# Optimization experiments

Measured on AMD Instinct MI355X. Metric: run time of the kernel, lower is better.

Reference implementation:

```python
import jax, jax.numpy as jnp
import numpy as np

B, D, U = 4096, 2048, 2048

def hard_sigmoid(x):
    # keras hard_sigmoid: clip(0.2*x + 0.5, 0, 1)
    return jnp.clip(0.2 * x + 0.5, 0.0, 1.0)

def setup_inputs() -> dict:
    key = jax.random.key(0)
    k1, k2, k3, k4, k5 = jax.random.split(key, 5)
    return {
        "inputs": jax.random.normal(k1, (B, D), dtype=jnp.float32),
        "h_tm1": jax.random.normal(k2, (B, U), dtype=jnp.float32),
        "c_tm1": jax.random.normal(k3, (B, U), dtype=jnp.float32),
        "kernel": jax.random.normal(k4, (D, 4 * U), dtype=jnp.float32) * 0.02,
        "recurrent_kernel": jax.random.normal(k5, (U, 4 * U), dtype=jnp.float32) * 0.02,
    }

def reference(inputs, h_tm1, c_tm1, kernel, recurrent_kernel):
    u = kernel.shape[1] // 4
    # One fused GEMM each for input and recurrent paths (same math as 8 split GEMMs)
    z = inputs @ kernel + h_tm1 @ recurrent_kernel  # [B, 4U]
    z_i, z_f, z_c, z_o = jnp.split(z, 4, axis=1)
    i = hard_sigmoid(z_i)
    f = hard_sigmoid(z_f)
    c = f * c_tm1 + i * jnp.tanh(z_c)
    o = hard_sigmoid(z_o)
    h = o * jnp.tanh(c)
    return (h, h, c)
```

## Files before the change

### kernel.cpp

```cpp
#include <hip/hip_runtime.h>
#include <stdint.h>

typedef unsigned short u16;
typedef float f32x4 __attribute__((ext_vector_type(4)));
typedef __bf16 bf16x8 __attribute__((ext_vector_type(8)));

#define B_ 4096
#define D_ 2048
#define U_ 2048
#define K_ 4096
#define N_ 8192
#define NT_ 128

__device__ __forceinline__ u16 f32_bf16(float f) {
  uint32_t u = __float_as_uint(f);
  u += 0x7FFFu + ((u >> 16) & 1u);
  return (u16)(u >> 16);
}
__device__ __forceinline__ float hsig(float x) {
  return fminf(fmaxf(0.2f * x + 0.5f, 0.0f), 1.0f);
}
__device__ __forceinline__ float ftanh(float x) {
  x = fminf(fmaxf(x, -15.0f), 15.0f);
  float e = __expf(2.0f * x);
  return (e - 1.0f) / (e + 1.0f);
}
__device__ __forceinline__ void gload16(const void* g, void* l) {
  __builtin_amdgcn_global_load_lds(
      (const __attribute__((address_space(1))) void*)g,
      (__attribute__((address_space(3))) void*)l,
      16, 0, 0);
}

__global__ __launch_bounds__(256) void cast_a(const float* __restrict__ x,
                                              const float* __restrict__ h,
                                              u16* __restrict__ A) {
  int c = blockIdx.x * 256 + threadIdx.x;
  int m = c >> 9;
  int kc = (c & 511) << 3;
  const float* src = (kc < D_) ? (x + (size_t)m * D_ + kc)
                               : (h + (size_t)m * U_ + (kc - D_));
  float4 v0 = ((const float4*)src)[0];
  float4 v1 = ((const float4*)src)[1];
  u16 o[8] = { f32_bf16(v0.x), f32_bf16(v0.y), f32_bf16(v0.z), f32_bf16(v0.w),
               f32_bf16(v1.x), f32_bf16(v1.y), f32_bf16(v1.z), f32_bf16(v1.w) };
  *(uint4*)(A + (size_t)c * 8) = *(const uint4*)o;
}

__global__ __launch_bounds__(256) void cast_wt(const float* __restrict__ kern,
                                               const float* __restrict__ rker,
                                               u16* __restrict__ Wt) {
  __shared__ u16 sW[64][68];
  const int t = threadIdx.x;
  const int bx = blockIdx.x;
  const int by = blockIdx.y;
  const int k0 = by * 64;
  const float* src = (k0 < D_) ? kern : rker;
  const int krow0 = (k0 < D_) ? k0 : (k0 - D_);
#pragma unroll
  for (int i = 0; i < 4; ++i) {
    int c = i * 256 + t;
    int kl = c >> 4;
    int nq = c & 15;
    int g  = nq >> 2;
    int ul = (nq & 3) << 2;
    int n  = g * U_ + bx * 16 + ul;
    float4 v = *(const float4*)(src + (size_t)(krow0 + kl) * N_ + n);
    u16 p[4] = { f32_bf16(v.x), f32_bf16(v.y), f32_bf16(v.z), f32_bf16(v.w) };
    *(ushort4*)&sW[kl][g * 16 + ul] = *(const ushort4*)p;
  }
  __syncthreads();
#pragma unroll
  for (int j = 0; j < 2; ++j) {
    int c2 = j * 256 + t;
    int nl = c2 >> 3;
    int kc = c2 & 7;
    u16 p[8];
#pragma unroll
    for (int jj = 0; jj < 8; ++jj) p[jj] = sW[kc * 8 + jj][nl];
    *(uint4*)(Wt + ((size_t)bx * 64 + nl) * K_ + k0 + kc * 8) = *(const uint4*)p;
  }
}

#define LDSA(par) ((par) * 32768)
#define LDSB(par) ((par) * 32768 + 16384)

#define STAGE4(par, t) do { \
  const u16* ga_ = Ab + (size_t)grow * K_ + (t) * 32 + gch8; \
  const u16* gb_ = Bb + (size_t)grow * K_ + (t) * 32 + gch8; \
  char* la_ = ldsc + LDSA(par) + wid * 1024; \
  char* lb_ = ldsc + LDSB(par) + wid * 1024; \
  gload16(ga_, la_); \
  gload16(ga_ + (size_t)128 * K_, la_ + 8192); \
  gload16(gb_, lb_); \
  gload16(gb_ + (size_t)128 * K_, lb_ + 8192); \
} while (0)

#define VMW(n) asm volatile("s_waitcnt vmcnt(" #n ")" ::: "memory")
#define MFMA16 __builtin_amdgcn_mfma_f32_16x16x32_bf16

#define PHASE(par, STAGE_STMT, VMW_STMT) do { \
  const char* pa_ = ldsc + LDSA(par) + aob; \
  const char* pb_ = ldsc + LDSB(par) + bob; \
  _Pragma("unroll") \
  for (int m_ = 0; m_ < 8; ++m_) av[m_] = *(const bf16x8*)(pa_ + m_ * 1024); \
  _Pragma("unroll") \
  for (int n_ = 0; n_ < 4; ++n_) bv[n_] = *(const bf16x8*)(pb_ + n_ * 1024); \
  STAGE_STMT; \
  VMW_STMT; \
  __builtin_amdgcn_s_barrier(); \
  asm volatile("s_waitcnt lgkmcnt(0)" ::: "memory"); \
  __builtin_amdgcn_sched_barrier(0); \
  __builtin_amdgcn_s_setprio(1); \
  _Pragma("unroll") \
  for (int m_ = 0; m_ < 8; ++m_) { \
    _Pragma("unroll") \
    for (int n_ = 0; n_ < 4; ++n_) \
      acc[m_][n_] = MFMA16(av[m_], bv[n_], acc[m_][n_], 0, 0, 0); \
  } \
  __builtin_amdgcn_s_setprio(0); \
} while (0)

__global__ __launch_bounds__(512, 2) void lstm_gemm(const u16* __restrict__ A,
                                                    const u16* __restrict__ Wt,
                                                    const float* __restrict__ c_prev,
                                                    float* __restrict__ out) {
  __shared__ __align__(16) u16 lds[65536];
  char* ldsc = (char*)lds;
  const int tid  = threadIdx.x;
  const int lane = tid & 63;
  const int wid  = tid >> 6;
  const int wr   = wid >> 2;
  const int wcn  = wid & 3;
  const int fr   = lane & 15;
  const int fq   = lane >> 4;

  const int orig = blockIdx.x;
  const int wg   = ((orig & 7) << 6) | (orig >> 3);
  const int bm   = wg & 15;
  const int bn   = wg >> 4;

  const u16* Ab = A  + (size_t)bm * 256 * K_;
  const u16* Bb = Wt + (size_t)bn * 256 * K_;

  const int grow = tid >> 2;
  const int gch8 = (((tid & 3) ^ ((grow >> 1) & 3)) << 3);
  const int csw = (fq ^ ((fr >> 1) & 3)) << 4;
  const int aob = (wr * 128 + fr) * 64 + csw;
  const int bob = (wcn * 64 + fr) * 64 + csw;

  f32x4 acc[8][4] = {};
  bf16x8 av[8], bv[4];

  STAGE4(0, 0);
  STAGE4(1, 1);
  VMW(4);
  __builtin_amdgcn_s_barrier();

  for (int tb = 0; tb < NT_; tb += 4) {
    PHASE(0, { STAGE4(2, tb + 2); }, { VMW(4); });
    PHASE(1, { STAGE4(3, tb + 3); }, { VMW(4); });
    PHASE(2, { if (tb + 4 < NT_) STAGE4(0, tb + 4); },
          { if (tb + 4 < NT_) { VMW(4); } else { VMW(0); } });
    PHASE(3, { if (tb + 5 < NT_) STAGE4(1, tb + 5); },
          { if (tb + 5 < NT_) { VMW(4); } });
  }

  const int u  = (bn * 4 + wcn) * 16 + fr;
  const size_t BU = (size_t)B_ * U_;
#pragma unroll
  for (int mi = 0; mi < 8; ++mi) {
#pragma unroll
    for (int r = 0; r < 4; ++r) {
      int row = bm * 256 + wr * 128 + mi * 16 + fq * 4 + r;
      float zi = acc[mi][0][r], zf = acc[mi][1][r];
      float zc = acc[mi][2][r], zo = acc[mi][3][r];
      float iv = hsig(zi), fv = hsig(zf), ov = hsig(zo);
      size_t off = (size_t)row * U_ + u;
      float cp = c_prev[off];
      float cv = fv * cp + iv * ftanh(zc);
      float hv = ov * ftanh(cv);
      out[off]          = hv;
      out[BU + off]     = hv;
      out[2 * BU + off] = cv;
    }
  }
}

extern "C" void kernel_launch(void* const* d_in, const int* in_sizes, int n_in,
                              void* d_out, int out_size, void* d_ws, size_t ws_size,
                              hipStream_t stream) {
  const float* x  = (const float*)d_in[0];
  const float* h  = (const float*)d_in[1];
  const float* cp = (const float*)d_in[2];
  const float* kk = (const float*)d_in[3];
  const float* rk = (const float*)d_in[4];
  float* out = (float*)d_out;

  const size_t bytesA  = (size_t)B_ * K_ * 2;
  const size_t bytesWt = (size_t)N_ * K_ * 2;
  if (ws_size < bytesA + bytesWt) return;

  u16* Aws = (u16*)d_ws;
  u16* Wt  = (u16*)((char*)d_ws + bytesA);

  cast_a<<<(B_ * K_ / 8) / 256, 256, 0, stream>>>(x, h, Aws);
  cast_wt<<<dim3(N_ / 64, K_ / 64), 256, 0, stream>>>(kk, rk, Wt);
  lstm_gemm<<<dim3(512), dim3(512), 0, stream>>>(Aws, Wt, cp, out);
}
```

Before: 305.7 us.

## Retile LSTM GEMM to 128x256 blocks with 4 waves and triple-buffered LDS

The GEMM block tile changes from 256x256 with 8 waves to 128x256 with 4 waves, launching 1024 blocks of 256 threads. Each wave now computes a 64x128 tile holding 32-wide gate slices, and cast_wt is rewritten to produce the matching 128-column gate interleave. The LDS pipeline moves from four buffers to three, with the barrier placed at the start of each phase and the LDS wait after the MFMAs. This aims to raise occupancy and overlap LDS reads with compute, at the cost of more A-tile reloads and more total blocks.

```diff
diff --git a/kernel.cpp b/kernel.cpp
--- a/kernel.cpp
+++ b/kernel.cpp
@@ -50,7 +50,7 @@
 __global__ __launch_bounds__(256) void cast_wt(const float* __restrict__ kern,
                                                const float* __restrict__ rker,
                                                u16* __restrict__ Wt) {
-  __shared__ u16 sW[64][68];
+  __shared__ u16 sW[64][134];
   const int t = threadIdx.x;
   const int bx = blockIdx.x;
   const int by = blockIdx.y;
@@ -58,131 +58,142 @@
   const float* src = (k0 < D_) ? kern : rker;
   const int krow0 = (k0 < D_) ? k0 : (k0 - D_);
 #pragma unroll
-  for (int i = 0; i < 4; ++i) {
-    int c = i * 256 + t;
-    int kl = c >> 4;
-    int nq = c & 15;
-    int g  = nq >> 2;
-    int ul = (nq & 3) << 2;
-    int n  = g * U_ + bx * 16 + ul;
+  for (int i = 0; i < 8; ++i) {
+    int q  = i * 256 + t;
+    int kl = q >> 5;
+    int cc = q & 31;
+    int g  = cc >> 3;
+    int n  = g * U_ + bx * 32 + (cc & 7) * 4;
     float4 v = *(const float4*)(src + (size_t)(krow0 + kl) * N_ + n);
     u16 p[4] = { f32_bf16(v.x), f32_bf16(v.y), f32_bf16(v.z), f32_bf16(v.w) };
-    *(ushort4*)&sW[kl][g * 16 + ul] = *(const ushort4*)p;
+    *(ushort4*)&sW[kl][cc * 4] = *(const ushort4*)p;
   }
   __syncthreads();
 #pragma unroll
-  for (int j = 0; j < 2; ++j) {
+  for (int j = 0; j < 4; ++j) {
     int c2 = j * 256 + t;
-    int nl = c2 >> 3;
+    int r  = c2 >> 3;
     int kc = c2 & 7;
     u16 p[8];
 #pragma unroll
-    for (int jj = 0; jj < 8; ++jj) p[jj] = sW[kc * 8 + jj][nl];
-    *(uint4*)(Wt + ((size_t)bx * 64 + nl) * K_ + k0 + kc * 8) = *(const uint4*)p;
-  }
-}
-
-#define LDSA(par) ((par) * 32768)
-#define LDSB(par) ((par) * 32768 + 16384)
-
-#define STAGE4(par, t) do { \
+    for (int jj = 0; jj < 8; ++jj) p[jj] = sW[kc * 8 + jj][r];
+    *(uint4*)(Wt + ((size_t)bx * 128 + r) * K_ + k0 + kc * 8) = *(const uint4*)p;
+  }
+}
+
+#define PA(par) ((par) * 24576)
+#define PB(par) ((par) * 24576 + 8192)
+
+#define STAGE6(par, t) do { \
   const u16* ga_ = Ab + (size_t)grow * K_ + (t) * 32 + gch8; \
   const u16* gb_ = Bb + (size_t)grow * K_ + (t) * 32 + gch8; \
-  char* la_ = ldsc + LDSA(par) + wid * 1024; \
-  char* lb_ = ldsc + LDSB(par) + wid * 1024; \
-  gload16(ga_, la_); \
-  gload16(ga_ + (size_t)128 * K_, la_ + 8192); \
-  gload16(gb_, lb_); \
+  char* la_ = ldsc + PA(par) + wid * 1024; \
+  char* lb_ = ldsc + PB(par) + wid * 1024; \
+  gload16(ga_,                    la_); \
+  gload16(ga_ + (size_t)64 * K_,  la_ + 4096); \
+  gload16(gb_,                    lb_); \
+  gload16(gb_ + (size_t)64 * K_,  lb_ + 4096); \
   gload16(gb_ + (size_t)128 * K_, lb_ + 8192); \
+  gload16(gb_ + (size_t)192 * K_, lb_ + 12288); \
 } while (0)
 
 #define VMW(n) asm volatile("s_waitcnt vmcnt(" #n ")" ::: "memory")
 #define MFMA16 __builtin_amdgcn_mfma_f32_16x16x32_bf16
 
 #define PHASE(par, STAGE_STMT, VMW_STMT) do { \
-  const char* pa_ = ldsc + LDSA(par) + aob; \
-  const char* pb_ = ldsc + LDSB(par) + bob; \
-  _Pragma("unroll") \
-  for (int m_ = 0; m_ < 8; ++m_) av[m_] = *(const bf16x8*)(pa_ + m_ * 1024); \
-  _Pragma("unroll") \
-  for (int n_ = 0; n_ < 4; ++n_) bv[n_] = *(const bf16x8*)(pb_ + n_ * 1024); \
+  __builtin_amdgcn_s_barrier(); \
+  asm volatile("" ::: "memory"); \
+  const char* pa_ = ldsc + PA(par) + aob; \
+  const char* pb_ = ldsc + PB(par) + bob; \
+  av[0] = *(const bf16x8*)(pa_); \
+  bv[0] = *(const bf16x8*)(pb_); \
+  bv[1] = *(const bf16x8*)(pb_ + 1024); \
+  bv[2] = *(const bf16x8*)(pb_ + 2048); \
+  bv[3] = *(const bf16x8*)(pb_ + 3072); \
+  bv[4] = *(const bf16x8*)(pb_ + 4096); \
+  bv[5] = *(const bf16x8*)(pb_ + 5120); \
+  bv[6] = *(const bf16x8*)(pb_ + 6144); \
+  bv[7] = *(const bf16x8*)(pb_ + 7168); \
+  av[1] = *(const bf16x8*)(pa_ + 1024); \
+  av[2] = *(const bf16x8*)(pa_ + 2048); \
+  av[3] = *(const bf16x8*)(pa_ + 3072); \
   STAGE_STMT; \
   VMW_STMT; \
-  __builtin_amdgcn_s_barrier(); \
-  asm volatile("s_waitcnt lgkmcnt(0)" ::: "memory"); \
-  __builtin_amdgcn_sched_barrier(0); \
   __builtin_amdgcn_s_setprio(1); \
   _Pragma("unroll") \
-  for (int m_ = 0; m_ < 8; ++m_) { \
+  for (int m_ = 0; m_ < 4; ++m_) { \
     _Pragma("unroll") \
-    for (int n_ = 0; n_ < 4; ++n_) \
+    for (int n_ = 0; n_ < 8; ++n_) \
       acc[m_][n_] = MFMA16(av[m_], bv[n_], acc[m_][n_], 0, 0, 0); \
   } \
   __builtin_amdgcn_s_setprio(0); \
+  asm volatile("s_waitcnt lgkmcnt(0)" ::: "memory"); \
 } while (0)
 
-__global__ __launch_bounds__(512, 2) void lstm_gemm(const u16* __restrict__ A,
+__global__ __launch_bounds__(256, 2) void lstm_gemm(const u16* __restrict__ A,
                                                     const u16* __restrict__ Wt,
                                                     const float* __restrict__ c_prev,
                                                     float* __restrict__ out) {
-  __shared__ __align__(16) u16 lds[65536];
+  __shared__ __align__(16) u16 lds[36864];
   char* ldsc = (char*)lds;
   const int tid  = threadIdx.x;
   const int lane = tid & 63;
   const int wid  = tid >> 6;
-  const int wr   = wid >> 2;
-  const int wcn  = wid & 3;
+  const int wr   = wid >> 1;
+  const int wcn  = wid & 1;
   const int fr   = lane & 15;
   const int fq   = lane >> 4;
 
   const int orig = blockIdx.x;
-  const int wg   = ((orig & 7) << 6) | (orig >> 3);
-  const int bm   = wg & 15;
-  const int bn   = wg >> 4;
-
-  const u16* Ab = A  + (size_t)bm * 256 * K_;
+  const int wg   = ((orig & 7) << 7) | (orig >> 3);
+  const int bm   = wg & 31;
+  const int bn   = wg >> 5;
+
+  const u16* Ab = A  + (size_t)bm * 128 * K_;
   const u16* Bb = Wt + (size_t)bn * 256 * K_;
 
   const int grow = tid >> 2;
   const int gch8 = (((tid & 3) ^ ((grow >> 1) & 3)) << 3);
   const int csw = (fq ^ ((fr >> 1) & 3)) << 4;
-  const int aob = (wr * 128 + fr) * 64 + csw;
-  const int bob = (wcn * 64 + fr) * 64 + csw;
-
-  f32x4 acc[8][4] = {};
-  bf16x8 av[8], bv[4];
-
-  STAGE4(0, 0);
-  STAGE4(1, 1);
-  VMW(4);
-  __builtin_amdgcn_s_barrier();
-
-  for (int tb = 0; tb < NT_; tb += 4) {
-    PHASE(0, { STAGE4(2, tb + 2); }, { VMW(4); });
-    PHASE(1, { STAGE4(3, tb + 3); }, { VMW(4); });
-    PHASE(2, { if (tb + 4 < NT_) STAGE4(0, tb + 4); },
-          { if (tb + 4 < NT_) { VMW(4); } else { VMW(0); } });
-    PHASE(3, { if (tb + 5 < NT_) STAGE4(1, tb + 5); },
-          { if (tb + 5 < NT_) { VMW(4); } });
-  }
-
-  const int u  = (bn * 4 + wcn) * 16 + fr;
+  const int aob = (wr * 64 + fr) * 64 + csw;
+  const int bob = (wcn * 128 + fr) * 64 + csw;
+
+  f32x4 acc[4][8] = {};
+  bf16x8 av[4], bv[8];
+
+  STAGE6(0, 0);
+  STAGE6(1, 1);
+  VMW(6);
+
+  for (int tb = 0; tb < 126; tb += 3) {
+    PHASE(0, { STAGE6(2, tb + 2); }, { VMW(6); });
+    PHASE(1, { STAGE6(0, tb + 3); }, { VMW(6); });
+    PHASE(2, { STAGE6(1, tb + 4); }, { VMW(6); });
+  }
+  PHASE(0, {}, { VMW(0); });
+  PHASE(1, {}, {});
+
+  const int ub = (bn * 2 + wcn) * 32;
   const size_t BU = (size_t)B_ * U_;
 #pragma unroll
-  for (int mi = 0; mi < 8; ++mi) {
-#pragma unroll
-    for (int r = 0; r < 4; ++r) {
-      int row = bm * 256 + wr * 128 + mi * 16 + fq * 4 + r;
-      float zi = acc[mi][0][r], zf = acc[mi][1][r];
-      float zc = acc[mi][2][r], zo = acc[mi][3][r];
-      float iv = hsig(zi), fv = hsig(zf), ov = hsig(zo);
-      size_t off = (size_t)row * U_ + u;
-      float cp = c_prev[off];
-      float cv = fv * cp + iv * ftanh(zc);
-      float hv = ov * ftanh(cv);
-      out[off]          = hv;
-      out[BU + off]     = hv;
-      out[2 * BU + off] = cv;
+  for (int mi = 0; mi < 4; ++mi) {
+#pragma unroll
+    for (int h = 0; h < 2; ++h) {
+#pragma unroll
+      for (int r = 0; r < 4; ++r) {
+        int row = bm * 128 + wr * 64 + mi * 16 + fq * 4 + r;
+        int u   = ub + h * 16 + fr;
+        float zi = acc[mi][0 + h][r], zf = acc[mi][2 + h][r];
+        float zc = acc[mi][4 + h][r], zo = acc[mi][6 + h][r];
+        float iv = hsig(zi), fv = hsig(zf), ov = hsig(zo);
+        size_t off = (size_t)row * U_ + u;
+        float cp = c_prev[off];
+        float cv = fv * cp + iv * ftanh(zc);
+        float hv = ov * ftanh(cv);
+        out[off]          = hv;
+        out[BU + off]     = hv;
+        out[2 * BU + off] = cv;
+      }
     }
   }
 }
@@ -205,6 +216,6 @@
   u16* Wt  = (u16*)((char*)d_ws + bytesA);
 
   cast_a<<<(B_ * K_ / 8) / 256, 256, 0, stream>>>(x, h, Aws);
-  cast_wt<<<dim3(N_ / 64, K_ / 64), 256, 0, stream>>>(kk, rk, Wt);
-  lstm_gemm<<<dim3(512), dim3(512), 0, stream>>>(Aws, Wt, cp, out);
-}
+  cast_wt<<<dim3(64, 64), 256, 0, stream>>>(kk, rk, Wt);
+  lstm_gemm<<<dim3(1024), dim3(256), 0, stream>>>(Aws, Wt, cp, out);
+}
```

Result: slower. 329.9 us (+7.9%).
